# Optimization experiments

Measured on AMD Instinct MI355X. Metric: run time of the kernel, lower is better.

Reference implementation:

```python
import jax, jax.numpy as jnp
import numpy as np

B, T, D, H = 32, 4096, 512, 8
HD = D // H
SCALE = HD ** -0.5


def setup_inputs() -> dict:
    key = jax.random.key(0)
    ks = jax.random.split(key, 5)
    s = 0.02
    return {
        "enc": jax.random.normal(ks[0], (B, T, D), dtype=jnp.float32),
        "Wq": jax.random.normal(ks[1], (D, D), dtype=jnp.float32) * s,
        "Wk": jax.random.normal(ks[2], (D, D), dtype=jnp.float32) * s,
        "Wv": jax.random.normal(ks[3], (D, D), dtype=jnp.float32) * s,
        "Wo": jax.random.normal(ks[4], (D, D), dtype=jnp.float32) * s,
    }


def reference(enc, Wq, Wk, Wv, Wo):
    b, t, d = enc.shape
    # projections (torch Linear: y = x @ W.T)
    q = enc[:, -1, :] @ Wq.T                     # [B, D]
    k = (enc @ Wk.T).reshape(b, t, H, HD)        # [B, T, H, HD]
    v = (enc @ Wv.T).reshape(b, t, H, HD)        # [B, T, H, HD]
    q = q.reshape(b, H, HD)                      # [B, H, HD]
    scores = jnp.einsum('bhd,bthd->bht', q, k) * SCALE   # [B, H, T]
    weights = jax.nn.softmax(scores, axis=-1)             # [B, H, T]
    context = jnp.einsum('bht,bthd->bhd', weights, v)     # [B, H, HD]
    context = context.reshape(b, d) @ Wo.T                # [B, D]
    return (context, weights.mean(axis=1))
```

## Files before the change

kernel.cpp:

```cpp
#include <hip/hip_runtime.h>

#define BB 32
#define TT 4096
#define DD 512
#define HH 8
#define HDD 64
#define SCALE_F 0.125f
#define CHUNKS 16
#define TC 256
#define RW 64

template<int CTRL>
__device__ __forceinline__ float dpp_add(float x) {
    int t = __builtin_amdgcn_update_dpp(0, __float_as_int(x), CTRL, 0xf, 0xf, true);
    return x + __int_as_float(t);
}

__global__ __launch_bounds__(256) void k_qu(const float* __restrict__ enc,
                                            const float* __restrict__ Wq,
                                            const float* __restrict__ Wk,
                                            float* __restrict__ u) {
    __shared__ float x[DD];
    __shared__ float qh[HDD];
    int b = blockIdx.x >> 3, h = blockIdx.x & 7;
    int tid = threadIdx.x;
    const float* el = enc + ((size_t)b * TT + (TT - 1)) * DD;
    for (int i = tid; i < DD; i += 256) x[i] = el[i];
    __syncthreads();
    if (tid < HDD) {
        const float4* wr = (const float4*)(Wq + (size_t)(h * HDD + tid) * DD);
        float acc = 0.f;
#pragma unroll 4
        for (int d = 0; d < DD / 4; ++d) {
            float4 w = wr[d];
            acc += w.x * x[4 * d] + w.y * x[4 * d + 1] + w.z * x[4 * d + 2] + w.w * x[4 * d + 3];
        }
        qh[tid] = acc;
    }
    __syncthreads();
#pragma unroll
    for (int k = 0; k < 2; ++k) {
        int d = tid + 256 * k;
        float acc = 0.f;
#pragma unroll 8
        for (int j = 0; j < HDD; ++j)
            acc += qh[j] * Wk[(size_t)(h * HDD + j) * DD + d];
        u[(size_t)(b * HH + h) * DD + d] = acc * SCALE_F;
    }
}

__global__ __launch_bounds__(256) void k_main(const float* __restrict__ enc,
                                              const float* __restrict__ u,
                                              float* __restrict__ wt,
                                              float* __restrict__ lsum,
                                              float* __restrict__ partial) {
    __shared__ float red[4][HH][DD];
    __shared__ float ls[HH];
    int b = blockIdx.x / CHUNKS, c = blockIdx.x % CHUNKS;
    int t0 = c * TC;
    int tid = threadIdx.x, wave = tid >> 6, lane = tid & 63;
    if (tid < HH) ls[tid] = 0.f;
    __syncthreads();

    const float* ub = u + (size_t)b * HH * DD;
    float4 uA[HH], uB[HH];
#pragma unroll
    for (int h = 0; h < HH; ++h) {
        uA[h] = *(const float4*)(ub + h * DD + 4 * lane);
        uB[h] = *(const float4*)(ub + h * DD + 256 + 4 * lane);
    }

    float4 accA[HH], accB[HH];
#pragma unroll
    for (int h = 0; h < HH; ++h) {
        accA[h] = make_float4(0.f, 0.f, 0.f, 0.f);
        accB[h] = make_float4(0.f, 0.f, 0.f, 0.f);
    }
    float Lacc[HH];
#pragma unroll
    for (int h = 0; h < HH; ++h) Lacc[h] = 0.f;

    int trow = t0 + wave * RW;
    const float* rp = enc + ((size_t)b * TT + trow) * DD;
    float* wp = wt + ((size_t)(b * HH + (lane & 7)) * TT) + trow;
    bool st = lane < HH;
    bool m1 = (lane & 1) != 0, m2 = (lane & 2) != 0, m4 = (lane & 4) != 0;

    float4 c0 = *(const float4*)(rp + 4 * lane);
    float4 c1 = *(const float4*)(rp + 256 + 4 * lane);
    float4 d0 = *(const float4*)(rp + DD + 4 * lane);
    float4 d1 = *(const float4*)(rp + DD + 256 + 4 * lane);

    for (int i = 0; i < RW; ++i) {
        float4 e0 = c0, e1 = c1;
        c0 = d0; c1 = d1;
        if (i + 2 < RW) {
            const float* np = rp + (size_t)(i + 2) * DD;
            d0 = *(const float4*)(np + 4 * lane);
            d1 = *(const float4*)(np + 256 + 4 * lane);
        }
        float a[HH];
#pragma unroll
        for (int h = 0; h < HH; ++h)
            a[h] = uA[h].x * e0.x + uA[h].y * e0.y + uA[h].z * e0.z + uA[h].w * e0.w
                 + uB[h].x * e1.x + uB[h].y * e1.y + uB[h].z * e1.z + uB[h].w * e1.w;
#pragma unroll
        for (int h = 0; h < HH; ++h) {
            a[h] = dpp_add<0xB1>(a[h]);
            a[h] = dpp_add<0x4E>(a[h]);
            a[h] = dpp_add<0x141>(a[h]);
            a[h] = dpp_add<0x128>(a[h]);
        }
#pragma unroll
        for (int h = 0; h < HH; ++h) a[h] += __shfl_xor(a[h], 16, 64);
#pragma unroll
        for (int h = 0; h < HH; ++h) a[h] += __shfl_xor(a[h], 32, 64);
        float wv[HH];
#pragma unroll
        for (int h = 0; h < HH; ++h) { wv[h] = __expf(a[h]); Lacc[h] += wv[h]; }
        {
            float s01 = m1 ? wv[1] : wv[0], s23 = m1 ? wv[3] : wv[2];
            float s45 = m1 ? wv[5] : wv[4], s67 = m1 ? wv[7] : wv[6];
            float sA = m2 ? s23 : s01, sB = m2 ? s67 : s45;
            float ws = m4 ? sB : sA;
            if (st) wp[i] = ws;
        }
#pragma unroll
        for (int h = 0; h < HH; ++h) {
            accA[h].x += wv[h] * e0.x; accA[h].y += wv[h] * e0.y;
            accA[h].z += wv[h] * e0.z; accA[h].w += wv[h] * e0.w;
            accB[h].x += wv[h] * e1.x; accB[h].y += wv[h] * e1.y;
            accB[h].z += wv[h] * e1.z; accB[h].w += wv[h] * e1.w;
        }
    }

#pragma unroll
    for (int h = 0; h < HH; ++h) {
        *(float4*)&red[wave][h][4 * lane] = accA[h];
        *(float4*)&red[wave][h][256 + 4 * lane] = accB[h];
    }
    if (lane == 0) {
#pragma unroll
        for (int h = 0; h < HH; ++h) atomicAdd(&ls[h], Lacc[h]);
    }
    __syncthreads();
    {
        int h = tid >> 5, col = (tid & 31) * 4;
        float* pb = partial + ((size_t)(b * CHUNKS + c) * HH + h) * DD;
#pragma unroll
        for (int j = 0; j < 4; ++j) {
            float4 r0 = *(const float4*)&red[0][h][col + 128 * j];
            float4 r1 = *(const float4*)&red[1][h][col + 128 * j];
            float4 r2 = *(const float4*)&red[2][h][col + 128 * j];
            float4 r3 = *(const float4*)&red[3][h][col + 128 * j];
            float4 o = make_float4(r0.x + r1.x + r2.x + r3.x,
                                   r0.y + r1.y + r2.y + r3.y,
                                   r0.z + r1.z + r2.z + r3.z,
                                   r0.w + r1.w + r2.w + r3.w);
            *(float4*)(pb + col + 128 * j) = o;
        }
    }
    if (tid < HH) lsum[(size_t)(b * CHUNKS + c) * HH + tid] = ls[tid];
}

__global__ __launch_bounds__(256) void k_vctx(const float* __restrict__ partial,
                                              const float* __restrict__ lsum,
                                              const float* __restrict__ Wv,
                                              float* __restrict__ ctxv) {
    __shared__ float cs[DD];
    __shared__ float Linv;
    int b = blockIdx.x >> 3, h = blockIdx.x & 7;
    int tid = threadIdx.x;
    if (tid == 0) {
        float L = 0.f;
#pragma unroll 8
        for (int c = 0; c < CHUNKS; ++c) L += lsum[(size_t)(b * CHUNKS + c) * HH + h];
        Linv = 1.0f / L;
    }
    float a0 = 0.f, a1 = 0.f;
    const float* pb = partial + (size_t)(b * CHUNKS) * HH * DD + (size_t)h * DD;
#pragma unroll 8
    for (int c = 0; c < CHUNKS; ++c) {
        const float* pp = pb + (size_t)c * HH * DD;
        a0 += pp[tid]; a1 += pp[tid + 256];
    }
    __syncthreads();
    cs[tid] = a0 * Linv; cs[tid + 256] = a1 * Linv;
    __syncthreads();
    int out = tid >> 2, q = tid & 3;
    int i = h * HDD + out;
    const float4* wr = (const float4*)(Wv + (size_t)i * DD + q * 128);
    const float* cc = cs + q * 128;
    float acc = 0.f;
#pragma unroll 8
    for (int d = 0; d < 32; ++d) {
        float4 w = wr[d];
        acc += w.x * cc[4 * d] + w.y * cc[4 * d + 1] + w.z * cc[4 * d + 2] + w.w * cc[4 * d + 3];
    }
    acc += __shfl_xor(acc, 1, 64);
    acc += __shfl_xor(acc, 2, 64);
    if (q == 0) ctxv[(size_t)b * DD + i] = acc;
}

__global__ __launch_bounds__(256) void k_o(const float* __restrict__ ctxv,
                                           const float* __restrict__ Wo,
                                           float* __restrict__ out0) {
    __shared__ float cs[DD];
    int b = blockIdx.x >> 3, g = blockIdx.x & 7;
    int tid = threadIdx.x;
    for (int i = tid; i < DD; i += 256) cs[i] = ctxv[(size_t)b * DD + i];
    __syncthreads();
    int out = tid >> 2, q = tid & 3;
    int o = g * HDD + out;
    const float4* wr = (const float4*)(Wo + (size_t)o * DD + q * 128);
    const float* cc = cs + q * 128;
    float acc = 0.f;
#pragma unroll 8
    for (int d = 0; d < 32; ++d) {
        float4 w = wr[d];
        acc += w.x * cc[4 * d] + w.y * cc[4 * d + 1] + w.z * cc[4 * d + 2] + w.w * cc[4 * d + 3];
    }
    acc += __shfl_xor(acc, 1, 64);
    acc += __shfl_xor(acc, 2, 64);
    if (q == 0) out0[(size_t)b * DD + o] = acc;
}

__global__ __launch_bounds__(256) void k_out1(const float* __restrict__ wt,
                                              const float* __restrict__ lsum,
                                              float* __restrict__ out1) {
    __shared__ float Linv[HH];
    int b = blockIdx.x >> 3, seg = blockIdx.x & 7;
    int tid = threadIdx.x;
    if (tid < HH) {
        float s = 0.f;
#pragma unroll 8
        for (int c = 0; c < CHUNKS; ++c) s += lsum[(size_t)(b * CHUNKS + c) * HH + tid];
        Linv[tid] = 0.125f / s;
    }
    __syncthreads();
#pragma unroll
    for (int k = 0; k < 2; ++k) {
        int t = seg * 512 + tid + 256 * k;
        float s = 0.f;
#pragma unroll
        for (int h = 0; h < HH; ++h)
            s += wt[(size_t)(b * HH + h) * TT + t] * Linv[h];
        out1[(size_t)b * TT + t] = s;
    }
}

extern "C" void kernel_launch(void* const* d_in, const int* in_sizes, int n_in,
                              void* d_out, int out_size, void* d_ws, size_t ws_size,
                              hipStream_t stream) {
    const float* enc = (const float*)d_in[0];
    const float* Wq  = (const float*)d_in[1];
    const float* Wk  = (const float*)d_in[2];
    const float* Wv  = (const float*)d_in[3];
    const float* Wo  = (const float*)d_in[4];

    float* ws = (float*)d_ws;
    float* u       = ws;
    float* wt      = u + (size_t)BB * HH * DD;
    float* lsum    = wt + (size_t)BB * HH * TT;
    float* partial = lsum + (size_t)BB * CHUNKS * HH;
    float* ctxv    = partial + (size_t)BB * CHUNKS * HH * DD;

    float* out0 = (float*)d_out;
    float* out1 = out0 + BB * DD;

    hipLaunchKernelGGL(k_qu,    dim3(BB * HH),     dim3(256), 0, stream, enc, Wq, Wk, u);
    hipLaunchKernelGGL(k_main,  dim3(BB * CHUNKS), dim3(256), 0, stream, enc, u, wt, lsum, partial);
    hipLaunchKernelGGL(k_vctx,  dim3(BB * HH),     dim3(256), 0, stream, partial, lsum, Wv, ctxv);
    hipLaunchKernelGGL(k_o,     dim3(BB * HH),     dim3(256), 0, stream, ctxv, Wo, out0);
    hipLaunchKernelGGL(k_out1,  dim3(BB * HH),     dim3(256), 0, stream, wt, lsum, out1);
}
```

Before: 410.2 us.

## Process two rows per iteration with deeper prefetch and merge tail kernels

```diff
diff --git a/kernel.cpp b/kernel.cpp
--- a/kernel.cpp
+++ b/kernel.cpp
@@ -14,6 +14,28 @@
 __device__ __forceinline__ float dpp_add(float x) {
     int t = __builtin_amdgcn_update_dpp(0, __float_as_int(x), CTRL, 0xf, 0xf, true);
     return x + __int_as_float(t);
+}
+
+__device__ __forceinline__ void row_weights(const float4* uA, const float4* uB,
+                                            float4 e0, float4 e1, float* wv) {
+    float a[HH];
+#pragma unroll
+    for (int h = 0; h < HH; ++h)
+        a[h] = uA[h].x * e0.x + uA[h].y * e0.y + uA[h].z * e0.z + uA[h].w * e0.w
+             + uB[h].x * e1.x + uB[h].y * e1.y + uB[h].z * e1.z + uB[h].w * e1.w;
+#pragma unroll
+    for (int h = 0; h < HH; ++h) {
+        a[h] = dpp_add<0xB1>(a[h]);
+        a[h] = dpp_add<0x4E>(a[h]);
+        a[h] = dpp_add<0x141>(a[h]);
+        a[h] = dpp_add<0x128>(a[h]);
+    }
+#pragma unroll
+    for (int h = 0; h < HH; ++h) a[h] += __shfl_xor(a[h], 16, 64);
+#pragma unroll
+    for (int h = 0; h < HH; ++h) a[h] += __shfl_xor(a[h], 32, 64);
+#pragma unroll
+    for (int h = 0; h < HH; ++h) wv[h] = __expf(a[h]);
 }
 
 __global__ __launch_bounds__(256) void k_qu(const float* __restrict__ enc,
@@ -86,52 +108,57 @@
     bool st = lane < HH;
     bool m1 = (lane & 1) != 0, m2 = (lane & 2) != 0, m4 = (lane & 4) != 0;
 
-    float4 c0 = *(const float4*)(rp + 4 * lane);
-    float4 c1 = *(const float4*)(rp + 256 + 4 * lane);
-    float4 d0 = *(const float4*)(rp + DD + 4 * lane);
-    float4 d1 = *(const float4*)(rp + DD + 256 + 4 * lane);
-
-    for (int i = 0; i < RW; ++i) {
-        float4 e0 = c0, e1 = c1;
-        c0 = d0; c1 = d1;
-        if (i + 2 < RW) {
-            const float* np = rp + (size_t)(i + 2) * DD;
-            d0 = *(const float4*)(np + 4 * lane);
-            d1 = *(const float4*)(np + 256 + 4 * lane);
-        }
-        float a[HH];
-#pragma unroll
-        for (int h = 0; h < HH; ++h)
-            a[h] = uA[h].x * e0.x + uA[h].y * e0.y + uA[h].z * e0.z + uA[h].w * e0.w
-                 + uB[h].x * e1.x + uB[h].y * e1.y + uB[h].z * e1.z + uB[h].w * e1.w;
+    float4 p0a = *(const float4*)(rp + 4 * lane);
+    float4 p0b = *(const float4*)(rp + 256 + 4 * lane);
+    float4 p1a = *(const float4*)(rp + DD + 4 * lane);
+    float4 p1b = *(const float4*)(rp + DD + 256 + 4 * lane);
+    float4 q0a = *(const float4*)(rp + 2 * DD + 4 * lane);
+    float4 q0b = *(const float4*)(rp + 2 * DD + 256 + 4 * lane);
+    float4 q1a = *(const float4*)(rp + 3 * DD + 4 * lane);
+    float4 q1b = *(const float4*)(rp + 3 * DD + 256 + 4 * lane);
+
+    for (int i = 0; i < RW; i += 2) {
+        int r4 = (i + 4) & (RW - 1), r5 = (i + 5) & (RW - 1);
+        const float* np4 = rp + (size_t)r4 * DD;
+        const float* np5 = rp + (size_t)r5 * DD;
+        float4 n0a = *(const float4*)(np4 + 4 * lane);
+        float4 n0b = *(const float4*)(np4 + 256 + 4 * lane);
+        float4 n1a = *(const float4*)(np5 + 4 * lane);
+        float4 n1b = *(const float4*)(np5 + 256 + 4 * lane);
+
+        float wv0[HH], wv1[HH];
+        row_weights(uA, uB, p0a, p0b, wv0);
+        row_weights(uA, uB, p1a, p1b, wv1);
+
+#pragma unroll
+        for (int h = 0; h < HH; ++h) { Lacc[h] += wv0[h] + wv1[h]; }
+
+        {
+            float s01 = m1 ? wv0[1] : wv0[0], s23 = m1 ? wv0[3] : wv0[2];
+            float s45 = m1 ? wv0[5] : wv0[4], s67 = m1 ? wv0[7] : wv0[6];
+            float sA = m2 ? s23 : s01, sB = m2 ? s67 : s45;
+            float ws0 = m4 ? sB : sA;
+            float t01 = m1 ? wv1[1] : wv1[0], t23 = m1 ? wv1[3] : wv1[2];
+            float t45 = m1 ? wv1[5] : wv1[4], t67 = m1 ? wv1[7] : wv1[6];
+            float tA = m2 ? t23 : t01, tB = m2 ? t67 : t45;
+            float ws1 = m4 ? tB : tA;
+            if (st) { wp[i] = ws0; wp[i + 1] = ws1; }
+        }
+
 #pragma unroll
         for (int h = 0; h < HH; ++h) {
-            a[h] = dpp_add<0xB1>(a[h]);
-            a[h] = dpp_add<0x4E>(a[h]);
-            a[h] = dpp_add<0x141>(a[h]);
-            a[h] = dpp_add<0x128>(a[h]);
-        }
-#pragma unroll
-        for (int h = 0; h < HH; ++h) a[h] += __shfl_xor(a[h], 16, 64);
-#pragma unroll
-        for (int h = 0; h < HH; ++h) a[h] += __shfl_xor(a[h], 32, 64);
-        float wv[HH];
-#pragma unroll
-        for (int h = 0; h < HH; ++h) { wv[h] = __expf(a[h]); Lacc[h] += wv[h]; }
-        {
-            float s01 = m1 ? wv[1] : wv[0], s23 = m1 ? wv[3] : wv[2];
-            float s45 = m1 ? wv[5] : wv[4], s67 = m1 ? wv[7] : wv[6];
-            float sA = m2 ? s23 : s01, sB = m2 ? s67 : s45;
-            float ws = m4 ? sB : sA;
-            if (st) wp[i] = ws;
-        }
-#pragma unroll
-        for (int h = 0; h < HH; ++h) {
-            accA[h].x += wv[h] * e0.x; accA[h].y += wv[h] * e0.y;
-            accA[h].z += wv[h] * e0.z; accA[h].w += wv[h] * e0.w;
-            accB[h].x += wv[h] * e1.x; accB[h].y += wv[h] * e1.y;
-            accB[h].z += wv[h] * e1.z; accB[h].w += wv[h] * e1.w;
-        }
+            accA[h].x += wv0[h] * p0a.x + wv1[h] * p1a.x;
+            accA[h].y += wv0[h] * p0a.y + wv1[h] * p1a.y;
+            accA[h].z += wv0[h] * p0a.z + wv1[h] * p1a.z;
+            accA[h].w += wv0[h] * p0a.w + wv1[h] * p1a.w;
+            accB[h].x += wv0[h] * p0b.x + wv1[h] * p1b.x;
+            accB[h].y += wv0[h] * p0b.y + wv1[h] * p1b.y;
+            accB[h].z += wv0[h] * p0b.z + wv1[h] * p1b.z;
+            accB[h].w += wv0[h] * p0b.w + wv1[h] * p1b.w;
+        }
+
+        p0a = q0a; p0b = q0b; p1a = q1a; p1b = q1b;
+        q0a = n0a; q0b = n0b; q1a = n1a; q1b = n1b;
     }
 
 #pragma unroll
@@ -202,50 +229,51 @@
     if (q == 0) ctxv[(size_t)b * DD + i] = acc;
 }
 
-__global__ __launch_bounds__(256) void k_o(const float* __restrict__ ctxv,
-                                           const float* __restrict__ Wo,
-                                           float* __restrict__ out0) {
+__global__ __launch_bounds__(256) void k_tail(const float* __restrict__ ctxv,
+                                              const float* __restrict__ Wo,
+                                              const float* __restrict__ wt,
+                                              const float* __restrict__ lsum,
+                                              float* __restrict__ out0,
+                                              float* __restrict__ out1) {
     __shared__ float cs[DD];
-    int b = blockIdx.x >> 3, g = blockIdx.x & 7;
+    int idx = blockIdx.x;
     int tid = threadIdx.x;
-    for (int i = tid; i < DD; i += 256) cs[i] = ctxv[(size_t)b * DD + i];
-    __syncthreads();
-    int out = tid >> 2, q = tid & 3;
-    int o = g * HDD + out;
-    const float4* wr = (const float4*)(Wo + (size_t)o * DD + q * 128);
-    const float* cc = cs + q * 128;
-    float acc = 0.f;
-#pragma unroll 8
-    for (int d = 0; d < 32; ++d) {
-        float4 w = wr[d];
-        acc += w.x * cc[4 * d] + w.y * cc[4 * d + 1] + w.z * cc[4 * d + 2] + w.w * cc[4 * d + 3];
-    }
-    acc += __shfl_xor(acc, 1, 64);
-    acc += __shfl_xor(acc, 2, 64);
-    if (q == 0) out0[(size_t)b * DD + o] = acc;
-}
-
-__global__ __launch_bounds__(256) void k_out1(const float* __restrict__ wt,
-                                              const float* __restrict__ lsum,
-                                              float* __restrict__ out1) {
-    __shared__ float Linv[HH];
-    int b = blockIdx.x >> 3, seg = blockIdx.x & 7;
-    int tid = threadIdx.x;
-    if (tid < HH) {
-        float s = 0.f;
-#pragma unroll 8
-        for (int c = 0; c < CHUNKS; ++c) s += lsum[(size_t)(b * CHUNKS + c) * HH + tid];
-        Linv[tid] = 0.125f / s;
-    }
-    __syncthreads();
-#pragma unroll
-    for (int k = 0; k < 2; ++k) {
-        int t = seg * 512 + tid + 256 * k;
-        float s = 0.f;
-#pragma unroll
-        for (int h = 0; h < HH; ++h)
-            s += wt[(size_t)(b * HH + h) * TT + t] * Linv[h];
-        out1[(size_t)b * TT + t] = s;
+    if (idx < BB * HH) {
+        int b = idx >> 3, g = idx & 7;
+        for (int i = tid; i < DD; i += 256) cs[i] = ctxv[(size_t)b * DD + i];
+        __syncthreads();
+        int out = tid >> 2, q = tid & 3;
+        int o = g * HDD + out;
+        const float4* wr = (const float4*)(Wo + (size_t)o * DD + q * 128);
+        const float* cc = cs + q * 128;
+        float acc = 0.f;
+#pragma unroll 8
+        for (int d = 0; d < 32; ++d) {
+            float4 w = wr[d];
+            acc += w.x * cc[4 * d] + w.y * cc[4 * d + 1] + w.z * cc[4 * d + 2] + w.w * cc[4 * d + 3];
+        }
+        acc += __shfl_xor(acc, 1, 64);
+        acc += __shfl_xor(acc, 2, 64);
+        if (q == 0) out0[(size_t)b * DD + o] = acc;
+    } else {
+        idx -= BB * HH;
+        int b = idx >> 3, seg = idx & 7;
+        if (tid < HH) {
+            float s = 0.f;
+#pragma unroll 8
+            for (int c = 0; c < CHUNKS; ++c) s += lsum[(size_t)(b * CHUNKS + c) * HH + tid];
+            cs[tid] = 0.125f / s;
+        }
+        __syncthreads();
+#pragma unroll
+        for (int k = 0; k < 2; ++k) {
+            int t = seg * 512 + tid + 256 * k;
+            float s = 0.f;
+#pragma unroll
+            for (int h = 0; h < HH; ++h)
+                s += wt[(size_t)(b * HH + h) * TT + t] * cs[h];
+            out1[(size_t)b * TT + t] = s;
+        }
     }
 }
 
@@ -271,6 +299,5 @@
     hipLaunchKernelGGL(k_qu,    dim3(BB * HH),     dim3(256), 0, stream, enc, Wq, Wk, u);
     hipLaunchKernelGGL(k_main,  dim3(BB * CHUNKS), dim3(256), 0, stream, enc, u, wt, lsum, partial);
     hipLaunchKernelGGL(k_vctx,  dim3(BB * HH),     dim3(256), 0, stream, partial, lsum, Wv, ctxv);
-    hipLaunchKernelGGL(k_o,     dim3(BB * HH),     dim3(256), 0, stream, ctxv, Wo, out0);
-    hipLaunchKernelGGL(k_out1,  dim3(BB * HH),     dim3(256), 0, stream, wt, lsum, out1);
-}
+    hipLaunchKernelGGL(k_tail,  dim3(2 * BB * HH), dim3(256), 0, stream, ctxv, Wo, wt, lsum, out0, out1);
+}
```

Result: no change. 417.2 us (+1.7%).
